# Kernel tuning notes

Hardware: AMD Instinct MI355X
Metric: run time of the kernel (lower is better)

## Reference

```python
import jax, jax.numpy as jnp
import numpy as np

N_NODES = 50000
N_EDGES = 600000
DIM = 128


def setup_inputs() -> dict:
    key = jax.random.key(0)
    k1, k2, k3, k4, k5, k6 = jax.random.split(key, 6)
    return {
        "h_v": jax.random.normal(k1, (N_NODES, DIM), dtype=jnp.float32),
        "h_d": jax.random.normal(k2, (N_EDGES, DIM), dtype=jnp.float32),
        "W_pi": jax.random.normal(k3, (DIM, 1), dtype=jnp.float32) * (1.0 / np.sqrt(DIM)),
        "W_M": jax.random.normal(k4, (2 * DIM, 1), dtype=jnp.float32) * (1.0 / np.sqrt(2 * DIM)),
        "src": jax.random.randint(k5, (N_EDGES,), 0, N_NODES, dtype=jnp.int64) if jax.config.jax_enable_x64 else jax.random.randint(k5, (N_EDGES,), 0, N_NODES, dtype=jnp.int32),
        "dst": jax.random.randint(k6, (N_EDGES,), 0, N_NODES, dtype=jnp.int32),
    }


def reference(h_v, h_d, W_pi, W_M, src, dst):
    # Gather per-edge endpoint features: [E, dim]
    ft_s = h_v[src]
    ft_d = h_v[dst]
    prod = ft_s * ft_d                                   # u_mul_v
    # e = pi(src*dst*d): [E, 1]
    e = (prod * h_d) @ W_pi
    # mask = sigmoid(M(cat([src*dst, d]))): [E, 1]
    mask = jax.nn.sigmoid(jnp.concatenate([prod, h_d], axis=-1) @ W_M)
    logits = (e * mask)[:, 0]                            # [E]
    # edge_softmax grouped by destination node (DGL semantics)
    seg_max = jax.ops.segment_max(logits, dst, num_segments=N_NODES)
    ex = jnp.exp(logits - seg_max[dst])
    seg_sum = jax.ops.segment_sum(ex, dst, num_segments=N_NODES)
    a = ex / seg_sum[dst]                                # [E]
    # dropout_local is identity at inference
    # message m = ft_src * a; aggregate sum over incoming edges per dst node
    out = jax.ops.segment_sum(ft_s * a[:, None], dst, num_segments=N_NODES)
    return out
```

## Files before the change

### kernel.cpp

```cpp
#include <hip/hip_runtime.h>

#define NN 50000
#define NE 600000
#define DIM 128
#define NB 196


__global__ __launch_bounds__(256) void zero_counts_kernel(int* __restrict__ counts) {
    int i = blockIdx.x * 256 + threadIdx.x;
    if (i < NN) counts[i] = 0;
}

__global__ __launch_bounds__(256) void hist_kernel(const int* __restrict__ dst,
                                                   int* __restrict__ counts) {
    int e = blockIdx.x * 256 + threadIdx.x;
    if (e < NE) atomicAdd(&counts[dst[e]], 1);
}

__global__ __launch_bounds__(256) void scan_pass1_kernel(const int* __restrict__ counts,
                                                         int* __restrict__ offsets,
                                                         int* __restrict__ blockSums) {
    __shared__ int tmp[256];
    int tid = threadIdx.x;
    int i = blockIdx.x * 256 + tid;
    int v = (i < NN) ? counts[i] : 0;
    tmp[tid] = v;
    __syncthreads();
    #pragma unroll
    for (int off = 1; off < 256; off <<= 1) {
        int t = (tid >= off) ? tmp[tid - off] : 0;
        __syncthreads();
        tmp[tid] += t;
        __syncthreads();
    }
    int incl = tmp[tid];
    if (i < NN) offsets[i] = incl - v;
    if (tid == 255) blockSums[blockIdx.x] = incl;
}

__global__ __launch_bounds__(256) void scan_pass2_kernel(int* __restrict__ blockSums) {
    __shared__ int tmp[256];
    int tid = threadIdx.x;
    int v = (tid < NB) ? blockSums[tid] : 0;
    tmp[tid] = v;
    __syncthreads();
    #pragma unroll
    for (int off = 1; off < 256; off <<= 1) {
        int t = (tid >= off) ? tmp[tid - off] : 0;
        __syncthreads();
        tmp[tid] += t;
        __syncthreads();
    }
    if (tid < NB) blockSums[tid] = tmp[tid] - v;
}

__global__ __launch_bounds__(256) void scan_pass3_kernel(int* __restrict__ offsets,
                                                         const int* __restrict__ blockSums,
                                                         int* __restrict__ cursor) {
    int i = blockIdx.x * 256 + threadIdx.x;
    if (i < NN) {
        int o = offsets[i] + blockSums[i >> 8];
        offsets[i] = o;
        cursor[i] = o;
    }
    if (i == 0) offsets[NN] = NE;
}


__global__ __launch_bounds__(256) void edge_logits_fused_kernel(
    const float* __restrict__ h_v, const float* __restrict__ h_d,
    const float* __restrict__ W_pi, const float* __restrict__ W_M,
    const int* __restrict__ src, const int* __restrict__ dst,
    int* __restrict__ cursor, float2* __restrict__ pairs) {
    int idx = blockIdx.x * 256 + threadIdx.x;
    int e = idx >> 5;
    int lane32 = threadIdx.x & 31;
    if (e >= NE) return;
    int s = src[e];
    int d = dst[e];
    const float4 fs = ((const float4*)(h_v + (size_t)s * DIM))[lane32];
    const float4 fd = ((const float4*)(h_v + (size_t)d * DIM))[lane32];
    const float4 hd = ((const float4*)(h_d + (size_t)e * DIM))[lane32];
    const float4 wp = ((const float4*)W_pi)[lane32];
    const float4 m0 = ((const float4*)W_M)[lane32];
    const float4 m1 = ((const float4*)(W_M + DIM))[lane32];

    float px = fs.x * fd.x, py = fs.y * fd.y, pz = fs.z * fd.z, pw = fs.w * fd.w;
    float s1 = px * hd.x * wp.x + py * hd.y * wp.y + pz * hd.z * wp.z + pw * hd.w * wp.w;
    float s2 = px * m0.x + py * m0.y + pz * m0.z + pw * m0.w
             + hd.x * m1.x + hd.y * m1.y + hd.z * m1.z + hd.w * m1.w;

    #pragma unroll
    for (int off = 16; off > 0; off >>= 1) {
        s1 += __shfl_xor(s1, off, 64);
        s2 += __shfl_xor(s2, off, 64);
    }
    if (lane32 == 0) {
        float logit = s1 / (1.0f + __expf(-s2));
        float ex = __expf(logit);
        int pos = atomicAdd(&cursor[d], 1);
        pairs[pos] = make_float2(__int_as_float(s), ex);
    }
}


__global__ __launch_bounds__(256) void node_aggregate_kernel(
    const float* __restrict__ h_v,
    const int* __restrict__ offsets,
    const float2* __restrict__ pairs,
    float* __restrict__ out) {
    int node = (blockIdx.x * 256 + threadIdx.x) >> 6;
    int lane = threadIdx.x & 63;
    if (node >= NN) return;
    int half = lane >> 5;
    int l32 = lane & 31;
    int beg = offsets[node];
    int end = offsets[node + 1];

    float4 acc = make_float4(0.0f, 0.0f, 0.0f, 0.0f);
    float ssum = 0.0f;
    for (int k = beg + half; k < end; k += 2) {
        float2 p = pairs[k];
        int s = __float_as_int(p.x);
        float ex = p.y;
        const float4 v = ((const float4*)(h_v + (size_t)s * DIM))[l32];
        acc.x += v.x * ex;
        acc.y += v.y * ex;
        acc.z += v.z * ex;
        acc.w += v.w * ex;
        ssum += ex;
    }
    acc.x += __shfl_xor(acc.x, 32, 64);
    acc.y += __shfl_xor(acc.y, 32, 64);
    acc.z += __shfl_xor(acc.z, 32, 64);
    acc.w += __shfl_xor(acc.w, 32, 64);
    ssum  += __shfl_xor(ssum, 32, 64);

    if (half == 0) {
        float inv = (ssum > 0.0f) ? 1.0f / ssum : 0.0f;
        ((float4*)(out + (size_t)node * DIM))[l32] =
            make_float4(acc.x * inv, acc.y * inv, acc.z * inv, acc.w * inv);
    }
}


extern "C" void kernel_launch(void* const* d_in, const int* in_sizes, int n_in,
                              void* d_out, int out_size, void* d_ws, size_t ws_size,
                              hipStream_t stream) {
    const float* h_v  = (const float*)d_in[0];
    const float* h_d  = (const float*)d_in[1];
    const float* W_pi = (const float*)d_in[2];
    const float* W_M  = (const float*)d_in[3];
    const int*   src  = (const int*)d_in[4];
    const int*   dst  = (const int*)d_in[5];
    float* out = (float*)d_out;

    int* counts     = (int*)d_ws;
    int* offsets    = counts + NN;
    int* cursor     = offsets + NN + 1;
    int* blockSums  = cursor + NN;
    float2* pairs   = (float2*)(((uintptr_t)(blockSums + 256) + 7) & ~(uintptr_t)7);

    zero_counts_kernel<<<NB, 256, 0, stream>>>(counts);
    hist_kernel<<<(NE + 255) / 256, 256, 0, stream>>>(dst, counts);
    scan_pass1_kernel<<<NB, 256, 0, stream>>>(counts, offsets, blockSums);
    scan_pass2_kernel<<<1, 256, 0, stream>>>(blockSums);
    scan_pass3_kernel<<<NB, 256, 0, stream>>>(offsets, blockSums, cursor);
    edge_logits_fused_kernel<<<(NE * 32 + 255) / 256, 256, 0, stream>>>(
        h_v, h_d, W_pi, W_M, src, dst, cursor, pairs);
    node_aggregate_kernel<<<(NN * 64 + 255) / 256, 256, 0, stream>>>(
        h_v, offsets, pairs, out);
}
```

Before: 557.5 us.

## Fuse edge logit computation into per-destination aggregation after CSR scatter

Replaces the per-edge logit kernel with a lightweight scatter that stores (src, edge id) pairs sorted by destination. The node kernel then loads the destination feature once and computes each edge's logit and exp inline while accumulating. This avoids gathering source rows twice and reading destination rows per edge. In exchange, h_d rows are now read in destination order rather than streamed, and the reduction shuffles sit inside the serial per-node loop.

```diff
diff --git a/kernel.cpp b/kernel.cpp
--- a/kernel.cpp
+++ b/kernel.cpp
@@ -66,70 +66,62 @@
     if (i == 0) offsets[NN] = NE;
 }
 
-
-__global__ __launch_bounds__(256) void edge_logits_fused_kernel(
-    const float* __restrict__ h_v, const float* __restrict__ h_d,
-    const float* __restrict__ W_pi, const float* __restrict__ W_M,
-    const int* __restrict__ src, const int* __restrict__ dst,
-    int* __restrict__ cursor, float2* __restrict__ pairs) {
-    int idx = blockIdx.x * 256 + threadIdx.x;
-    int e = idx >> 5;
-    int lane32 = threadIdx.x & 31;
+__global__ __launch_bounds__(256) void scatter_kernel(const int* __restrict__ src,
+                                                      const int* __restrict__ dst,
+                                                      int* __restrict__ cursor,
+                                                      int2* __restrict__ pairs) {
+    int e = blockIdx.x * 256 + threadIdx.x;
     if (e >= NE) return;
-    int s = src[e];
     int d = dst[e];
-    const float4 fs = ((const float4*)(h_v + (size_t)s * DIM))[lane32];
-    const float4 fd = ((const float4*)(h_v + (size_t)d * DIM))[lane32];
-    const float4 hd = ((const float4*)(h_d + (size_t)e * DIM))[lane32];
-    const float4 wp = ((const float4*)W_pi)[lane32];
-    const float4 m0 = ((const float4*)W_M)[lane32];
-    const float4 m1 = ((const float4*)(W_M + DIM))[lane32];
-
-    float px = fs.x * fd.x, py = fs.y * fd.y, pz = fs.z * fd.z, pw = fs.w * fd.w;
-    float s1 = px * hd.x * wp.x + py * hd.y * wp.y + pz * hd.z * wp.z + pw * hd.w * wp.w;
-    float s2 = px * m0.x + py * m0.y + pz * m0.z + pw * m0.w
-             + hd.x * m1.x + hd.y * m1.y + hd.z * m1.z + hd.w * m1.w;
-
-    #pragma unroll
-    for (int off = 16; off > 0; off >>= 1) {
-        s1 += __shfl_xor(s1, off, 64);
-        s2 += __shfl_xor(s2, off, 64);
-    }
-    if (lane32 == 0) {
-        float logit = s1 / (1.0f + __expf(-s2));
-        float ex = __expf(logit);
-        int pos = atomicAdd(&cursor[d], 1);
-        pairs[pos] = make_float2(__int_as_float(s), ex);
-    }
+    int pos = atomicAdd(&cursor[d], 1);
+    pairs[pos] = make_int2(src[e], e);
 }
 
 
-__global__ __launch_bounds__(256) void node_aggregate_kernel(
-    const float* __restrict__ h_v,
-    const int* __restrict__ offsets,
-    const float2* __restrict__ pairs,
+__global__ __launch_bounds__(256) void node_fused_kernel(
+    const float* __restrict__ h_v, const float* __restrict__ h_d,
+    const float* __restrict__ W_pi, const float* __restrict__ W_M,
+    const int* __restrict__ offsets, const int2* __restrict__ pairs,
     float* __restrict__ out) {
     int node = (blockIdx.x * 256 + threadIdx.x) >> 6;
     int lane = threadIdx.x & 63;
     if (node >= NN) return;
     int half = lane >> 5;
     int l32 = lane & 31;
+
+    const float4 fd = ((const float4*)(h_v + (size_t)node * DIM))[l32];
+    const float4 wp = ((const float4*)W_pi)[l32];
+    const float4 m0 = ((const float4*)W_M)[l32];
+    const float4 m1 = ((const float4*)(W_M + DIM))[l32];
+
     int beg = offsets[node];
     int end = offsets[node + 1];
 
     float4 acc = make_float4(0.0f, 0.0f, 0.0f, 0.0f);
     float ssum = 0.0f;
     for (int k = beg + half; k < end; k += 2) {
-        float2 p = pairs[k];
-        int s = __float_as_int(p.x);
-        float ex = p.y;
-        const float4 v = ((const float4*)(h_v + (size_t)s * DIM))[l32];
-        acc.x += v.x * ex;
-        acc.y += v.y * ex;
-        acc.z += v.z * ex;
-        acc.w += v.w * ex;
+        int2 p = pairs[k];
+        const float4 fs = ((const float4*)(h_v + (size_t)p.x * DIM))[l32];
+        const float4 hd = ((const float4*)(h_d + (size_t)p.y * DIM))[l32];
+
+        float px = fs.x * fd.x, py = fs.y * fd.y, pz = fs.z * fd.z, pw = fs.w * fd.w;
+        float s1 = px * hd.x * wp.x + py * hd.y * wp.y + pz * hd.z * wp.z + pw * hd.w * wp.w;
+        float s2 = px * m0.x + py * m0.y + pz * m0.z + pw * m0.w
+                 + hd.x * m1.x + hd.y * m1.y + hd.z * m1.z + hd.w * m1.w;
+        #pragma unroll
+        for (int off = 16; off > 0; off >>= 1) {
+            s1 += __shfl_xor(s1, off, 64);
+            s2 += __shfl_xor(s2, off, 64);
+        }
+        float logit = s1 / (1.0f + __expf(-s2));
+        float ex = __expf(logit);
+        acc.x += fs.x * ex;
+        acc.y += fs.y * ex;
+        acc.z += fs.z * ex;
+        acc.w += fs.w * ex;
         ssum += ex;
     }
+
     acc.x += __shfl_xor(acc.x, 32, 64);
     acc.y += __shfl_xor(acc.y, 32, 64);
     acc.z += __shfl_xor(acc.z, 32, 64);
@@ -155,19 +147,18 @@
     const int*   dst  = (const int*)d_in[5];
     float* out = (float*)d_out;
 
-    int* counts     = (int*)d_ws;
-    int* offsets    = counts + NN;
-    int* cursor     = offsets + NN + 1;
-    int* blockSums  = cursor + NN;
-    float2* pairs   = (float2*)(((uintptr_t)(blockSums + 256) + 7) & ~(uintptr_t)7);
+    int* counts    = (int*)d_ws;
+    int* offsets   = counts + NN;
+    int* cursor    = offsets + NN + 1;
+    int* blockSums = cursor + NN;
+    int2* pairs    = (int2*)(((uintptr_t)(blockSums + 256) + 7) & ~(uintptr_t)7);
 
     zero_counts_kernel<<<NB, 256, 0, stream>>>(counts);
     hist_kernel<<<(NE + 255) / 256, 256, 0, stream>>>(dst, counts);
     scan_pass1_kernel<<<NB, 256, 0, stream>>>(counts, offsets, blockSums);
     scan_pass2_kernel<<<1, 256, 0, stream>>>(blockSums);
     scan_pass3_kernel<<<NB, 256, 0, stream>>>(offsets, blockSums, cursor);
-    edge_logits_fused_kernel<<<(NE * 32 + 255) / 256, 256, 0, stream>>>(
-        h_v, h_d, W_pi, W_M, src, dst, cursor, pairs);
-    node_aggregate_kernel<<<(NN * 64 + 255) / 256, 256, 0, stream>>>(
-        h_v, offsets, pairs, out);
+    scatter_kernel<<<(NE + 255) / 256, 256, 0, stream>>>(src, dst, cursor, pairs);
+    node_fused_kernel<<<(NN * 64 + 255) / 256, 256, 0, stream>>>(
+        h_v, h_d, W_pi, W_M, offsets, pairs, out);
 }
```

Measured after the change: 524.8 us. 1.06x faster.
